# Optimization experiments

Hardware: AMD Instinct MI355X
Metric: run time of the kernel (lower is better)

## Reference

```python
import jax, jax.numpy as jnp
import numpy as np

EPS = 1e-5  # F.layer_norm default eps
H_STEP = 0.1


def double_layer(x, K1, K2):
    # x: [1, Cin, N]; K1: [Cmid, Cin]; K2: [Cout, Cmid]  (1x1 conv1d == matmul)
    x = jnp.einsum('oc,bcn->bon', K1, x)
    # F.layer_norm(x, x.shape): normalize over the whole tensor, no affine
    m = jnp.mean(x)
    v = jnp.mean((x - m) ** 2)
    x = jnp.tanh((x - m) * jax.lax.rsqrt(v + EPS))
    return jnp.einsum('oc,bcn->bon', K2, x)


def setup_inputs() -> dict:
    key = jax.random.key(0)
    ks = jax.random.split(key, 12)
    N = 4096; nNin = 64; nopen = 256; nhid = 256; nNclose = 256
    nlayer = 8; num_output = 1024; E0 = 16 * N
    stdv = 1e-3
    return {
        'xn': jax.random.normal(ks[0], (1, nNin, N), jnp.float32),
        'K1Nopen': jax.random.normal(ks[1], (nopen, nNin), jnp.float32) * stdv,
        'K2Nopen': jax.random.normal(ks[2], (nopen, nopen), jnp.float32) * stdv,
        'KNclose': jax.random.normal(ks[3], (nNclose, nopen), jnp.float32) * stdv,
        'KN1': jax.random.uniform(ks[4], (nlayer, nhid, 2 * nopen), jnp.float32) * stdv,
        'KN2': jax.random.uniform(ks[5], (nlayer, nopen, nhid), jnp.float32) * stdv,
        'lin1_w': jax.random.normal(ks[6], (nopen, nopen), jnp.float32) / np.sqrt(nopen),
        'lin1_b': jnp.zeros((nopen,), jnp.float32),
        'lin2_w': jax.random.normal(ks[7], (num_output, nopen), jnp.float32) / np.sqrt(nopen),
        'lin2_b': jnp.zeros((num_output,), jnp.float32),
        'edge_i': jax.random.randint(ks[8], (E0,), 0, N),
        'edge_j': jax.random.randint(ks[9], (E0,), 0, N),
    }


def reference(xn, K1Nopen, K2Nopen, KNclose, KN1, KN2,
              lin1_w, lin1_b, lin2_w, lin2_b, edge_i, edge_j):
    N = xn.shape[-1]
    # gcn_norm's add_remaining_self_loops: input edge list has no self loops,
    # so append one per node once (fixed shapes; D[i,i] == exp(0) == 1 == fill).
    I = jnp.concatenate([edge_i, jnp.arange(N)])
    J = jnp.concatenate([edge_j, jnp.arange(N)])

    xn = double_layer(xn, K1Nopen, K2Nopen)  # [1, nopen, N]
    nlayers = KN1.shape[0]
    for i in range(nlayers):
        # --- updateGraph: dense pairwise Gaussian affinity, then gcn_norm ---
        f = xn[0]                          # [C, N]
        sq = jnp.sum(f * f, axis=0)        # [N]
        D = jax.nn.relu(sq[None, :] + sq[:, None] - 2.0 * (f.T @ f))  # [N, N]
        D = jnp.exp(-2.0 * (D / jnp.std(D, ddof=1)))
        w = D[I, J]                                          # gather edge affinities
        deg = jax.ops.segment_sum(w, J, num_segments=N)
        dis = jnp.where(deg > 0, jax.lax.rsqrt(deg), 0.0)
        W = dis[I] * w * dis[J]                              # normalized edge weights [E]
        # --- nodeLap = edgeDiv(nodeGrad(xn)) ---
        g = W[None, None, :] * (xn[:, :, I] - xn[:, :, J])   # nodeGrad [1, C, E]
        wg = (W[None, None, :] * g)[0].T                     # [E, C]
        lap = (jax.ops.segment_sum(wg, I, num_segments=N)
               - jax.ops.segment_sum(wg, J, num_segments=N)).T[None]  # [1, C, N]
        dxn = jnp.concatenate([xn, lap], axis=1)             # varlet features [1, 2C, N]
        dxn = double_layer(dxn, KN1[i], KN2[i])              # [1, C, N]
        xn = xn + H_STEP * dxn                               # heat update

    xn = jnp.einsum('oc,bcn->bon', KNclose, xn)[0].T         # [N, nNclose]
    x = jax.nn.elu(xn @ lin1_w.T + lin1_b)
    x = x @ lin2_w.T + lin2_b
    return jax.nn.log_softmax(x, axis=1)                     # [N, num_output]
```

## Files before the change

### kernel.cpp

```cpp
#include <hip/hip_runtime.h>
#include <hip/hip_bf16.h>

#define N_NODES 4096
#define CF      256
#define CIN     64
#define E0_EDGES 65536
#define NLAYER  8
#define NOUT    1024
#define CN      (CF * N_NODES)
#define STD_BLOCKS 64

typedef unsigned short ushort;
typedef __attribute__((ext_vector_type(8))) short s8v;
typedef __attribute__((ext_vector_type(4))) float f4v;

__device__ __forceinline__ ushort f2bf(float x){
  unsigned int u = __builtin_bit_cast(unsigned int, x);
  return (ushort)((u + 0x7FFFu + ((u >> 16) & 1u)) >> 16);
}
__device__ __forceinline__ float bf2f(ushort h){
  unsigned int u = ((unsigned int)h) << 16;
  return __builtin_bit_cast(float, u);
}

__device__ __forceinline__ float waveSumF(float v){
  #pragma unroll
  for (int o = 32; o; o >>= 1) v += __shfl_xor(v, o);
  return v;
}
__device__ __forceinline__ double waveSumD(double v){
  #pragma unroll
  for (int o = 32; o; o >>= 1) v += __shfl_xor(v, o);
  return v;
}
__device__ __forceinline__ float waveMaxF(float v){
  #pragma unroll
  for (int o = 32; o; o >>= 1) v = fmaxf(v, __shfl_xor(v, o));
  return v;
}
__device__ float blockSumF(float v){
  __shared__ float sm[4];
  v = waveSumF(v);
  int l = threadIdx.x & 63, w = threadIdx.x >> 6;
  __syncthreads();
  if (l == 0) sm[w] = v;
  __syncthreads();
  return sm[0] + sm[1] + sm[2] + sm[3];
}
__device__ double blockSumD(double v){
  __shared__ double sm[4];
  v = waveSumD(v);
  int l = threadIdx.x & 63, w = threadIdx.x >> 6;
  __syncthreads();
  if (l == 0) sm[w] = v;
  __syncthreads();
  return sm[0] + sm[1] + sm[2] + sm[3];
}
__device__ float blockMaxF(float v){
  __shared__ float sm[4];
  v = waveMaxF(v);
  int l = threadIdx.x & 63, w = threadIdx.x >> 6;
  __syncthreads();
  if (l == 0) sm[w] = v;
  __syncthreads();
  return fmaxf(fmaxf(sm[0], sm[1]), fmaxf(sm[2], sm[3]));
}

#define MF(a,b,c) c = __builtin_amdgcn_mfma_f32_16x16x32_bf16(a, b, c, 0, 0, 0)

template<int BK, int ACT, bool WF32, bool WBF, bool WFH, bool MV, bool TRI>
__global__ __launch_bounds__(256)
void gemmB1(const ushort* __restrict__ A1, const ushort* __restrict__ A2,
            int lda, int splitAt,
            const ushort* __restrict__ B, int ldb,
            float* __restrict__ Cf, ushort* __restrict__ Cb, ushort* __restrict__ Cfh,
            int ldc, size_t cStrideZ, int kChunk,
            float alpha, float beta, const float* __restrict__ bias,
            double* __restrict__ pS, double* __restrict__ pS2)
{
  constexpr int NC = BK / 32;
  __shared__ ushort As[2][64][BK + 8], Bs[2][64][BK + 8];
  const int tid = threadIdx.x;
  const int r  = tid >> 2;
  const int kq = (tid & 3) * (BK / 4);
  int bx = blockIdx.x, by = blockIdx.y;
  if (TRI) {
    const int trT[10] = {0,0,0,0,1,1,1,2,2,3};
    const int tcT[10] = {0,1,2,3,1,2,3,2,3,3};
    by = trT[blockIdx.x]; bx = tcT[blockIdx.x];
  }
  const int row0 = by * 64, col0 = bx * 64;
  const int kStart = blockIdx.z * kChunk;
  const int nT = kChunk / BK;

  const int wid = tid >> 6, lane = tid & 63;
  const int wr = (wid >> 1) * 32, wc = (wid & 1) * 32;
  const int fr = lane & 15, fk = (lane >> 4) * 8;

  f4v acc[2][2] = {};
  s8v rA0[NC], rB0[NC], rA1[NC], rB1[NC];

#define LOADTILE(T, RA, RB) { \
    int k0 = kStart + (T) * BK; \
    const ushort* Ag; int kk; \
    if (k0 < splitAt) { Ag = A1; kk = k0; } else { Ag = A2; kk = k0 - splitAt; } \
    size_t aoff = (size_t)(row0 + r) * lda + kk + kq; \
    size_t boff = (size_t)(col0 + r) * ldb + k0 + kq; \
    _Pragma("unroll") \
    for (int c = 0; c < NC; c++) { \
      RA[c] = *(const s8v*)(Ag + aoff + 8 * c); \
      RB[c] = *(const s8v*)(B + boff + 8 * c); } }

#define STORETILE(BUF, RA, RB) { \
    _Pragma("unroll") \
    for (int c = 0; c < NC; c++) { \
      *(s8v*)&As[BUF][r][kq + 8 * c] = RA[c]; \
      *(s8v*)&Bs[BUF][r][kq + 8 * c] = RB[c]; } }

#define MFMAT(BUF) { \
    _Pragma("unroll") \
    for (int ks = 0; ks < BK; ks += 32) { \
      s8v a0 = *(const s8v*)&As[BUF][wr + fr][ks + fk]; \
      s8v a1 = *(const s8v*)&As[BUF][wr + 16 + fr][ks + fk]; \
      s8v b0 = *(const s8v*)&Bs[BUF][wc + fr][ks + fk]; \
      s8v b1 = *(const s8v*)&Bs[BUF][wc + 16 + fr][ks + fk]; \
      MF(a0, b0, acc[0][0]); \
      MF(a0, b1, acc[0][1]); \
      MF(a1, b0, acc[1][0]); \
      MF(a1, b1, acc[1][1]); } }

  LOADTILE(0, rA0, rB0);
  if (nT > 1) LOADTILE(1, rA1, rB1);
  STORETILE(0, rA0, rB0);

  for (int t = 0; t < nT; t += 2) {
    __syncthreads();
    if (t + 2 < nT) LOADTILE(t + 2, rA0, rB0);
    MFMAT(0);
    if (t + 1 < nT) {
      STORETILE(1, rA1, rB1);
      __syncthreads();
      if (t + 3 < nT) LOADTILE(t + 3, rA1, rB1);
      MFMAT(1);
      if (t + 2 < nT) STORETILE(0, rA0, rB0);
    }
  }
#undef LOADTILE
#undef STORETILE
#undef MFMAT

  double s = 0, s2 = 0;
  #pragma unroll
  for (int m = 0; m < 2; m++)
    #pragma unroll
    for (int n = 0; n < 2; n++) {
      const int rowb = row0 + wr + m * 16 + (lane >> 4) * 4;
      const int col  = col0 + wc + n * 16 + fr;
      ushort4 hv;
      #pragma unroll
      for (int q = 0; q < 4; q++) {
        size_t cidx = (size_t)(rowb + q) * ldc + col;
        float v = alpha * acc[m][n][q];
        if (cStrideZ) {
          Cf[blockIdx.z * cStrideZ + cidx] = v;
        } else {
          if (beta != 0.0f) v += beta * Cf[cidx];
          if (bias) v += bias[col];
          if (ACT == 1) v = (v > 0.0f) ? v : expm1f(v);
          if (WF32) Cf[cidx] = v;
          if (WBF)  Cb[cidx] = f2bf(v);
          if (WFH)  ((ushort*)&hv)[q] = f2bf(v);
          if (MV)   { s += v; s2 += (double)v * v; }
        }
      }
      if (WFH && !cStrideZ)
        *(ushort4*)(Cfh + (size_t)col * N_NODES + rowb) = hv;
    }
  if (MV) {
    s  = blockSumD(s);
    s2 = blockSumD(s2);
    if (tid == 0) {
      int bid = blockIdx.y * gridDim.x + blockIdx.x;
      pS[bid] = s; pS2[bid] = s2;
    }
  }
}

#define OFF_K1   0
#define OFF_K2   16384
#define OFF_KNC  81920
#define OFF_KN1  147456
#define OFF_KN2  1196032
#define OFF_L1   1720320
#define OFF_L2   1785856
#define NW_TOT   2048000

__global__ __launch_bounds__(256)
void prepWK(const float* s0, const float* s1, const float* s2, const float* s3,
            const float* s4, const float* s5, const float* s6,
            ushort* __restrict__ h)
{
  const int sizes[7] = {16384, 65536, 65536, 1048576, 524288, 65536, 262144};
  const int offs[7]  = {OFF_K1, OFF_K2, OFF_KNC, OFF_KN1, OFF_KN2, OFF_L1, OFF_L2};
  int seg = blockIdx.y;
  const float* src = seg==0?s0: seg==1?s1: seg==2?s2: seg==3?s3: seg==4?s4: seg==5?s5: s6;
  int n = sizes[seg], off = offs[seg];
  for (int i = blockIdx.x * 256 + threadIdx.x; i < n; i += gridDim.x * 256)
    h[off + i] = f2bf(src[i]);
}

__global__ __launch_bounds__(256)
void transposeBF(const float* __restrict__ in, ushort* __restrict__ outh, int R, int Cc)
{
  __shared__ float t[32][33];
  int x  = blockIdx.x * 32 + threadIdx.x;
  int y0 = blockIdx.y * 32;
  for (int dy = threadIdx.y; dy < 32; dy += 8)
    t[dy][threadIdx.x] = in[(size_t)(y0 + dy) * Cc + x];
  __syncthreads();
  int ox  = y0 + threadIdx.x;
  int oy0 = blockIdx.x * 32;
  for (int dy = threadIdx.y; dy < 32; dy += 8)
    outh[(size_t)(oy0 + dy) * R + ox] = f2bf(t[threadIdx.x][dy]);
}

__global__ __launch_bounds__(256)
void tanhNormBF(ushort* __restrict__ h, const double* __restrict__ pS,
                const double* __restrict__ pS2)
{
  __shared__ float bc[2];
  double a = pS[threadIdx.x], b = pS2[threadIdx.x];
  a = blockSumD(a);
  b = blockSumD(b);
  if (threadIdx.x == 0) {
    double m   = a / (double)CN;
    double var = b / (double)CN - m * m;
    bc[0] = (float)m;
    bc[1] = (float)(1.0 / sqrt(var + 1e-5));
  }
  __syncthreads();
  float mf = bc[0], rs = bc[1];
  for (size_t i = ((size_t)blockIdx.x * 256 + threadIdx.x) * 8; i < CN;
       i += (size_t)256 * 256 * 8) {
    s8v hv = *(s8v*)(h + i);
    #pragma unroll
    for (int k = 0; k < 8; k++) {
      float x = bf2f((ushort)hv[k]);
      x = tanhf((x - mf) * rs);
      hv[k] = (short)f2bf(x);
    }
    *(s8v*)(h + i) = hv;
  }
}

__global__ __launch_bounds__(256)
void sqSHK(const ushort* __restrict__ fTh, float* __restrict__ sq,
           float* __restrict__ sP, float* __restrict__ hP, float* __restrict__ deg)
{
  __shared__ float smS[4][256], smH[4][256];
  int b = blockIdx.x, w = threadIdx.x >> 6, lane = threadIdx.x & 63;
  if (threadIdx.x < 64) deg[b * 64 + threadIdx.x] = 0.0f;
  float sA[4] = {0,0,0,0}, hA[4] = {0,0,0,0};
  for (int rr = 0; rr < 16; rr++) {
    int n = b * 64 + rr * 4 + w;
    ushort4 u = ((const ushort4*)(fTh + (size_t)n * CF))[lane];
    float x0 = bf2f(u.x), x1 = bf2f(u.y), x2 = bf2f(u.z), x3 = bf2f(u.w);
    float q = waveSumF(x0*x0 + x1*x1 + x2*x2 + x3*x3);
    if (lane == 0) sq[n] = q;
    sA[0] += x0; sA[1] += x1; sA[2] += x2; sA[3] += x3;
    hA[0] += x0*q; hA[1] += x1*q; hA[2] += x2*q; hA[3] += x3*q;
  }
  #pragma unroll
  for (int k = 0; k < 4; k++) { smS[w][lane*4+k] = sA[k]; smH[w][lane*4+k] = hA[k]; }
  __syncthreads();
  int t = threadIdx.x;
  sP[(size_t)b * 256 + t] = smS[0][t] + smS[1][t] + smS[2][t] + smS[3][t];
  hP[(size_t)b * 256 + t] = smH[0][t] + smH[1][t] + smH[2][t] + smH[3][t];
}

__global__ __launch_bounds__(256)
void stdPartsK(const float* __restrict__ sP, const float* __restrict__ hP,
               const float* __restrict__ Gp, const float* __restrict__ sq,
               double* __restrict__ parts)
{
  int b = blockIdx.x, t = threadIdx.x;
  double S1 = 0, S2 = 0, sd = 0, hd = 0, gf = 0;
  for (int i = b * 256 + t; i < N_NODES; i += STD_BLOCKS * 256) {
    double q = sq[i]; S1 += q; S2 += q * q;
  }
  if (b == 0) {
    float sv = 0, hv = 0;
    for (int p = 0; p < 64; p++) { sv += sP[p * 256 + t]; hv += hP[p * 256 + t]; }
    sd = (double)sv * sv; hd = (double)hv * sv;
  }
  for (int i = b * 256 + t; i < CF * CF; i += STD_BLOCKS * 256) {
    int r = i >> 8, c = i & 255;
    if (r > c) continue;
    double g = 0;
    #pragma unroll 4
    for (int z = 0; z < 16; z++) g += Gp[(size_t)z * 65536 + i];
    gf += (r == c) ? g * g : 2.0 * g * g;
  }
  S1 = blockSumD(S1);
  S2 = blockSumD(S2);
  sd = blockSumD(sd);
  hd = blockSumD(hd);
  gf = blockSumD(gf);
  if (t == 0) {
    parts[0 * STD_BLOCKS + b] = S1;
    parts[1 * STD_BLOCKS + b] = S2;
    parts[2 * STD_BLOCKS + b] = sd;
    parts[3 * STD_BLOCKS + b] = hd;
    parts[4 * STD_BLOCKS + b] = gf;
  }
}

__global__ __launch_bounds__(256)
void edgeWK(const int* __restrict__ ei, const int* __restrict__ ej,
            const ushort* __restrict__ fTh, const float* __restrict__ sq,
            const double* __restrict__ parts, float* __restrict__ wE,
            float* __restrict__ deg)
{
  __shared__ float c0s;
  if (threadIdx.x < 64) {
    int l = threadIdx.x;
    double v0 = waveSumD(parts[0 * STD_BLOCKS + l]);
    double v1 = waveSumD(parts[1 * STD_BLOCKS + l]);
    double v2 = waveSumD(parts[2 * STD_BLOCKS + l]);
    double v3 = waveSumD(parts[3 * STD_BLOCKS + l]);
    double v4 = waveSumD(parts[4 * STD_BLOCKS + l]);
    if (l == 0) {
      double NN = (double)N_NODES;
      double sum1 = 2.0 * NN * v0 - 2.0 * v2;
      double sum2 = 2.0 * NN * v1 + 2.0 * v0 * v0 + 4.0 * v4 - 8.0 * v3;
      double n2 = NN * NN;
      double var = (sum2 - sum1 * sum1 / n2) / (n2 - 1.0);
      double sdev = sqrt(var > 0 ? var : 0);
      c0s = (float)(-2.0 / sdev);
    }
  }
  __syncthreads();
  float c0 = c0s;
  int w = threadIdx.x >> 6, lane = threadIdx.x & 63;
  int e0 = (blockIdx.x * 4 + w) * 4;
  for (int q = 0; q < 4; q++) {
    int e = e0 + q;
    int i = ei[e], j = ej[e];
    ushort4 ua = ((const ushort4*)(fTh + (size_t)i * CF))[lane];
    ushort4 ub = ((const ushort4*)(fTh + (size_t)j * CF))[lane];
    float d = waveSumF(bf2f(ua.x)*bf2f(ub.x) + bf2f(ua.y)*bf2f(ub.y) +
                       bf2f(ua.z)*bf2f(ub.z) + bf2f(ua.w)*bf2f(ub.w));
    if (lane == 0) {
      float dist = fmaxf(sq[i] + sq[j] - 2.0f * d, 0.0f);
      float ww = expf(c0 * dist);
      wE[e] = ww;
      unsafeAtomicAdd(&deg[j], ww);
    }
  }
}

__global__ __launch_bounds__(256)
void wsqK(const int* __restrict__ ei, const int* __restrict__ ej,
          const float* __restrict__ wE, const float* __restrict__ deg,
          float* __restrict__ Wsq)
{
  int e = blockIdx.x * 256 + threadIdx.x;
  float W = rsqrtf(1.0f + deg[ei[e]]) * wE[e] * rsqrtf(1.0f + deg[ej[e]]);
  Wsq[e] = W * W;
}

__global__ __launch_bounds__(256)
void csrCountK(const int* __restrict__ ei, const int* __restrict__ ej,
               int* __restrict__ cntO, int* __restrict__ cntI)
{
  int e = blockIdx.x * 256 + threadIdx.x;
  atomicAdd(&cntO[ei[e]], 1);
  atomicAdd(&cntI[ej[e]], 1);
}

__global__ __launch_bounds__(256)
void csrScanK(const int* __restrict__ cntO, const int* __restrict__ cntI,
              int* __restrict__ ofsO, int* __restrict__ ofsI)
{
  __shared__ int smO[256], smI[256];
  int t = threadIdx.x;
  int lo[16], li[16];
  int sO = 0, sI = 0;
  #pragma unroll
  for (int k = 0; k < 16; k++) {
    lo[k] = cntO[t * 16 + k]; li[k] = cntI[t * 16 + k];
    sO += lo[k]; sI += li[k];
  }
  smO[t] = sO; smI[t] = sI;
  __syncthreads();
  for (int off = 1; off < 256; off <<= 1) {
    int aO = (t >= off) ? smO[t - off] : 0;
    int aI = (t >= off) ? smI[t - off] : 0;
    __syncthreads();
    smO[t] += aO; smI[t] += aI;
    __syncthreads();
  }
  int bO = smO[t] - sO;
  int bI = smI[t] - sI;
  #pragma unroll
  for (int k = 0; k < 16; k++) {
    ofsO[t * 16 + k] = bO; bO += lo[k];
    ofsI[t * 16 + k] = bI; bI += li[k];
  }
}

__global__ __launch_bounds__(256)
void csrFillK(const int* __restrict__ ei, const int* __restrict__ ej,
              const int* __restrict__ ofsO, const int* __restrict__ ofsI,
              int* __restrict__ curO, int* __restrict__ curI,
              int2* __restrict__ lstO, int2* __restrict__ lstI)
{
  int e = blockIdx.x * 256 + threadIdx.x;
  int i = ei[e], j = ej[e];
  int p = atomicAdd(&curO[i], 1); lstO[ofsO[i] + p] = make_int2(j, e);
  int q = atomicAdd(&curI[j], 1); lstI[ofsI[j] + q] = make_int2(i, e);
}

__global__ __launch_bounds__(256)
void gatherLapK(const int2* __restrict__ lstO, const int2* __restrict__ lstI,
                const int* __restrict__ ofsO, const int* __restrict__ ofsI,
                const int* __restrict__ cntO, const int* __restrict__ cntI,
                const float* __restrict__ Wsq,
                const ushort* __restrict__ fTh, ushort* __restrict__ lapTh)
{
  int w = threadIdx.x >> 6, lane = threadIdx.x & 63;
  int n = blockIdx.x * 4 + w;
  ushort4 u = ((const ushort4*)(fTh + (size_t)n * CF))[lane];
  float o0 = bf2f(u.x), o1 = bf2f(u.y), o2 = bf2f(u.z), o3 = bf2f(u.w);
  float a0 = 0, a1 = 0, a2 = 0, a3 = 0;
  int p0 = ofsO[n], pc = cntO[n];
  for (int k = 0; k < pc; k++) {
    int2 oe = lstO[p0 + k];
    float W2 = Wsq[oe.y];
    ushort4 v = ((const ushort4*)(fTh + (size_t)oe.x * CF))[lane];
    a0 += W2 * (o0 - bf2f(v.x)); a1 += W2 * (o1 - bf2f(v.y));
    a2 += W2 * (o2 - bf2f(v.z)); a3 += W2 * (o3 - bf2f(v.w));
  }
  int q0 = ofsI[n], qc = cntI[n];
  for (int k = 0; k < qc; k++) {
    int2 oe = lstI[q0 + k];
    float W2 = Wsq[oe.y];
    ushort4 v = ((const ushort4*)(fTh + (size_t)oe.x * CF))[lane];
    a0 += W2 * (o0 - bf2f(v.x)); a1 += W2 * (o1 - bf2f(v.y));
    a2 += W2 * (o2 - bf2f(v.z)); a3 += W2 * (o3 - bf2f(v.w));
  }
  ushort4 rv;
  rv.x = f2bf(a0); rv.y = f2bf(a1); rv.z = f2bf(a2); rv.w = f2bf(a3);
  ((ushort4*)(lapTh + (size_t)n * CF))[lane] = rv;
}

__global__ __launch_bounds__(256)
void logSoftmaxK(const float* __restrict__ logits, float* __restrict__ out)
{
  int n = blockIdx.x;
  const float* row = logits + (size_t)n * NOUT;
  float mx = -1e30f;
  for (int o = threadIdx.x; o < NOUT; o += 256) mx = fmaxf(mx, row[o]);
  mx = blockMaxF(mx);
  float se = 0;
  for (int o = threadIdx.x; o < NOUT; o += 256) se += expf(row[o] - mx);
  se = blockSumF(se);
  float lse = mx + logf(se);
  for (int o = threadIdx.x; o < NOUT; o += 256) out[(size_t)n * NOUT + o] = row[o] - lse;
}

extern "C" void kernel_launch(void* const* d_in, const int* in_sizes, int n_in,
                              void* d_out, int out_size, void* d_ws, size_t ws_size,
                              hipStream_t stream)
{
  (void)in_sizes; (void)n_in; (void)out_size; (void)ws_size;
  const float* x0      = (const float*)d_in[0];
  const float* K1      = (const float*)d_in[1];
  const float* K2      = (const float*)d_in[2];
  const float* KNclose = (const float*)d_in[3];
  const float* KN1     = (const float*)d_in[4];
  const float* KN2     = (const float*)d_in[5];
  const float* lin1w   = (const float*)d_in[6];
  const float* lin1b   = (const float*)d_in[7];
  const float* lin2w   = (const float*)d_in[8];
  const float* lin2b   = (const float*)d_in[9];
  const int*   ei      = (const int*)d_in[10];
  const int*   ej      = (const int*)d_in[11];
  float* out = (float*)d_out;

  float* base   = (float*)d_ws;
  float* fT     = base;
  float* logits = fT + (size_t)CN;
  float* Gp     = logits + 4 * (size_t)CN;
  float* sq     = Gp + (size_t)CN;
  float* deg    = sq + N_NODES;
  float* sP     = deg + N_NODES;
  float* hP     = sP + 64 * 256;
  float* wE     = hP + 64 * 256;
  float* Wsq    = wE + E0_EDGES;
  double* pS    = (double*)(Wsq + E0_EDGES + 2);
  double* pS2   = pS + 256;
  double* parts = pS2 + 256;

  ushort* u0 = (ushort*)(((uintptr_t)(parts + 5 * STD_BLOCKS) + 15) & ~(uintptr_t)15);
  ushort* fTh   = u0;
  ushort* fh    = fTh + (size_t)CN;
  ushort* lapTh = fh + (size_t)CN;
  ushort* uTh   = lapTh + (size_t)CN;
  ushort* wH    = uTh + (size_t)CN;
  int* ib = (int*)(((uintptr_t)(wH + NW_TOT) + 15) & ~(uintptr_t)15);
  int*  cntO = ib;
  int*  cntI = cntO + N_NODES;
  int*  ofsO = cntI + N_NODES;
  int*  ofsI = ofsO + N_NODES;
  int*  curO = ofsI + N_NODES;
  int*  curI = curO + N_NODES;
  int2* lstO = (int2*)(curI + N_NODES);
  int2* lstI = lstO + E0_EDGES;

  prepWK<<<dim3(64, 7), 256, 0, stream>>>(K1, K2, KNclose, KN1, KN2, lin1w, lin2w, wH);
  hipMemsetAsync(cntO, 0, 6 * N_NODES * sizeof(int), stream);
  csrCountK<<<E0_EDGES/256, 256, 0, stream>>>(ei, ej, cntO, cntI);
  csrScanK<<<1, 256, 0, stream>>>(cntO, cntI, ofsO, ofsI);
  csrFillK<<<E0_EDGES/256, 256, 0, stream>>>(ei, ej, ofsO, ofsI, curO, curI, lstO, lstI);

  transposeBF<<<dim3(N_NODES/32, CIN/32), dim3(32, 8), 0, stream>>>(x0, fh, CIN, N_NODES);
  gemmB1<64,0,0,1,0,1,false><<<dim3(4,64,1), 256, 0, stream>>>(
      fh, fh, CIN, 1 << 30, wH + OFF_K1, CIN,
      nullptr, uTh, nullptr, CF, 0, CIN, 1.f, 0.f, nullptr, pS, pS2);
  tanhNormBF<<<256, 256, 0, stream>>>(uTh, pS, pS2);
  gemmB1<128,0,1,1,1,0,false><<<dim3(4,64,1), 256, 0, stream>>>(
      uTh, uTh, CF, 1 << 30, wH + OFF_K2, CF,
      fT, fTh, fh, CF, 0, CF, 1.f, 0.f, nullptr, nullptr, nullptr);

  for (int L = 0; L < NLAYER; L++) {
    const ushort* k1h = wH + OFF_KN1 + (size_t)L * CF * 2 * CF;
    const ushort* k2h = wH + OFF_KN2 + (size_t)L * CF * CF;

    sqSHK<<<64, 256, 0, stream>>>(fTh, sq, sP, hP, deg);
    gemmB1<128,0,1,0,0,0,true><<<dim3(10,1,16), 256, 0, stream>>>(
        fh, fh, N_NODES, 1 << 30, fh, N_NODES,
        Gp, nullptr, nullptr, CF, 65536, 256, 1.f, 0.f, nullptr, nullptr, nullptr);
    stdPartsK<<<STD_BLOCKS, 256, 0, stream>>>(sP, hP, Gp, sq, parts);
    edgeWK<<<E0_EDGES/16, 256, 0, stream>>>(ei, ej, fTh, sq, parts, wE, deg);
    wsqK<<<E0_EDGES/256, 256, 0, stream>>>(ei, ej, wE, deg, Wsq);
    gatherLapK<<<N_NODES/4, 256, 0, stream>>>(lstO, lstI, ofsO, ofsI, cntO, cntI,
                                              Wsq, fTh, lapTh);
    gemmB1<128,0,0,1,0,1,false><<<dim3(4,64,1), 256, 0, stream>>>(
        fTh, lapTh, CF, 256, k1h, 2*CF,
        nullptr, uTh, nullptr, CF, 0, 2*CF, 1.f, 0.f, nullptr, pS, pS2);
    tanhNormBF<<<256, 256, 0, stream>>>(uTh, pS, pS2);
    gemmB1<128,0,1,1,1,0,false><<<dim3(4,64,1), 256, 0, stream>>>(
        uTh, uTh, CF, 1 << 30, k2h, CF,
        fT, fTh, fh, CF, 0, CF, 0.1f, 1.f, nullptr, nullptr, nullptr);
  }

  gemmB1<128,0,0,1,0,0,false><<<dim3(4,64,1), 256, 0, stream>>>(
      fTh, fTh, CF, 1 << 30, wH + OFF_KNC, CF,
      nullptr, uTh, nullptr, CF, 0, CF, 1.f, 0.f, nullptr, nullptr, nullptr);
  gemmB1<128,1,0,1,0,0,false><<<dim3(4,64,1), 256, 0, stream>>>(
      uTh, uTh, CF, 1 << 30, wH + OFF_L1, CF,
      nullptr, lapTh, nullptr, CF, 0, CF, 1.f, 0.f, lin1b, nullptr, nullptr);
  gemmB1<128,0,1,0,0,0,false><<<dim3(16,64,1), 256, 0, stream>>>(
      lapTh, lapTh, CF, 1 << 30, wH + OFF_L2, CF,
      logits, nullptr, nullptr, NOUT, 0, CF, 1.f, 0.f, lin2b, nullptr, nullptr);
  logSoftmaxK<<<N_NODES, 256, 0, stream>>>(logits, out);
}
```

Before: 820.7 us.

## Fuse tanh-norm into GEMM load, atomic split-K Gram, coarser edge kernel

Removes the standalone tanhNormBF pass by applying the layer-norm tanh while staging A tiles into shared memory of the following GEMM; each block recomputes mean/var from the partial sums. The split-K Gram GEMM now accumulates into a single 256x256 buffer with atomics (zeroed in sqSHK) instead of writing 16 partial slabs that stdPartsK summed. The edge weight kernel processes 16 edges per wave with fewer blocks. Tradeoffs: tanh is recomputed for each column tile (4x redundancy), atomics make the sum order nondeterministic, and edgeWK has less parallelism.

```diff
diff --git a/kernel.cpp b/kernel.cpp
--- a/kernel.cpp
+++ b/kernel.cpp
@@ -68,7 +68,8 @@
 
 #define MF(a,b,c) c = __builtin_amdgcn_mfma_f32_16x16x32_bf16(a, b, c, 0, 0, 0)
 
-template<int BK, int ACT, bool WF32, bool WBF, bool WFH, bool MV, bool TRI>
+template<int BK, int ACT, bool WF32, bool WBF, bool WFH, bool MV, bool TRI,
+         bool TANH, bool ATO>
 __global__ __launch_bounds__(256)
 void gemmB1(const ushort* __restrict__ A1, const ushort* __restrict__ A2,
             int lda, int splitAt,
@@ -97,6 +98,17 @@
   const int wr = (wid >> 1) * 32, wc = (wid & 1) * 32;
   const int fr = lane & 15, fk = (lane >> 4) * 8;
 
+  float mf = 0.0f, rs = 0.0f;
+  if (TANH) {
+    double a = pS[tid], b = pS2[tid];
+    a = blockSumD(a);
+    b = blockSumD(b);
+    double m   = a / (double)CN;
+    double var = b / (double)CN - m * m;
+    mf = (float)m;
+    rs = (float)(1.0 / sqrt(var + 1e-5));
+  }
+
   f4v acc[2][2] = {};
   s8v rA0[NC], rB0[NC], rA1[NC], rB1[NC];
 
@@ -114,7 +126,13 @@
 #define STORETILE(BUF, RA, RB) { \
     _Pragma("unroll") \
     for (int c = 0; c < NC; c++) { \
-      *(s8v*)&As[BUF][r][kq + 8 * c] = RA[c]; \
+      s8v av = RA[c]; \
+      if (TANH) { \
+        _Pragma("unroll") \
+        for (int k2 = 0; k2 < 8; k2++) { \
+          float x = bf2f((ushort)av[k2]); \
+          av[k2] = (short)f2bf(tanhf((x - mf) * rs)); } } \
+      *(s8v*)&As[BUF][r][kq + 8 * c] = av; \
       *(s8v*)&Bs[BUF][r][kq + 8 * c] = RB[c]; } }
 
 #define MFMAT(BUF) { \
@@ -161,7 +179,9 @@
       for (int q = 0; q < 4; q++) {
         size_t cidx = (size_t)(rowb + q) * ldc + col;
         float v = alpha * acc[m][n][q];
-        if (cStrideZ) {
+        if (ATO) {
+          unsafeAtomicAdd(&Cf[cidx], v);
+        } else if (cStrideZ) {
           Cf[blockIdx.z * cStrideZ + cidx] = v;
         } else {
           if (beta != 0.0f) v += beta * Cf[cidx];
@@ -173,7 +193,7 @@
           if (MV)   { s += v; s2 += (double)v * v; }
         }
       }
-      if (WFH && !cStrideZ)
+      if (WFH && !cStrideZ && !ATO)
         *(ushort4*)(Cfh + (size_t)col * N_NODES + rowb) = hv;
     }
   if (MV) {
@@ -225,41 +245,14 @@
 }
 
 __global__ __launch_bounds__(256)
-void tanhNormBF(ushort* __restrict__ h, const double* __restrict__ pS,
-                const double* __restrict__ pS2)
-{
-  __shared__ float bc[2];
-  double a = pS[threadIdx.x], b = pS2[threadIdx.x];
-  a = blockSumD(a);
-  b = blockSumD(b);
-  if (threadIdx.x == 0) {
-    double m   = a / (double)CN;
-    double var = b / (double)CN - m * m;
-    bc[0] = (float)m;
-    bc[1] = (float)(1.0 / sqrt(var + 1e-5));
-  }
-  __syncthreads();
-  float mf = bc[0], rs = bc[1];
-  for (size_t i = ((size_t)blockIdx.x * 256 + threadIdx.x) * 8; i < CN;
-       i += (size_t)256 * 256 * 8) {
-    s8v hv = *(s8v*)(h + i);
-    #pragma unroll
-    for (int k = 0; k < 8; k++) {
-      float x = bf2f((ushort)hv[k]);
-      x = tanhf((x - mf) * rs);
-      hv[k] = (short)f2bf(x);
-    }
-    *(s8v*)(h + i) = hv;
-  }
-}
-
-__global__ __launch_bounds__(256)
 void sqSHK(const ushort* __restrict__ fTh, float* __restrict__ sq,
-           float* __restrict__ sP, float* __restrict__ hP, float* __restrict__ deg)
+           float* __restrict__ sP, float* __restrict__ hP,
+           float* __restrict__ deg, float* __restrict__ G)
 {
   __shared__ float smS[4][256], smH[4][256];
   int b = blockIdx.x, w = threadIdx.x >> 6, lane = threadIdx.x & 63;
   if (threadIdx.x < 64) deg[b * 64 + threadIdx.x] = 0.0f;
+  ((float4*)G)[b * 256 + threadIdx.x] = make_float4(0.f, 0.f, 0.f, 0.f);
   float sA[4] = {0,0,0,0}, hA[4] = {0,0,0,0};
   for (int rr = 0; rr < 16; rr++) {
     int n = b * 64 + rr * 4 + w;
@@ -280,7 +273,7 @@
 
 __global__ __launch_bounds__(256)
 void stdPartsK(const float* __restrict__ sP, const float* __restrict__ hP,
-               const float* __restrict__ Gp, const float* __restrict__ sq,
+               const float* __restrict__ G, const float* __restrict__ sq,
                double* __restrict__ parts)
 {
   int b = blockIdx.x, t = threadIdx.x;
@@ -296,9 +289,7 @@
   for (int i = b * 256 + t; i < CF * CF; i += STD_BLOCKS * 256) {
     int r = i >> 8, c = i & 255;
     if (r > c) continue;
-    double g = 0;
-    #pragma unroll 4
-    for (int z = 0; z < 16; z++) g += Gp[(size_t)z * 65536 + i];
+    double g = G[i];
     gf += (r == c) ? g * g : 2.0 * g * g;
   }
   S1 = blockSumD(S1);
@@ -342,8 +333,8 @@
   __syncthreads();
   float c0 = c0s;
   int w = threadIdx.x >> 6, lane = threadIdx.x & 63;
-  int e0 = (blockIdx.x * 4 + w) * 4;
-  for (int q = 0; q < 4; q++) {
+  int e0 = (blockIdx.x * 4 + w) * 16;
+  for (int q = 0; q < 16; q++) {
     int e = e0 + q;
     int i = ei[e], j = ej[e];
     ushort4 ua = ((const ushort4*)(fTh + (size_t)i * CF))[lane];
@@ -491,8 +482,8 @@
   float* base   = (float*)d_ws;
   float* fT     = base;
   float* logits = fT + (size_t)CN;
-  float* Gp     = logits + 4 * (size_t)CN;
-  float* sq     = Gp + (size_t)CN;
+  float* G      = logits + 4 * (size_t)CN;
+  float* sq     = G + CF * CF;
   float* deg    = sq + N_NODES;
   float* sP     = deg + N_NODES;
   float* hP     = sP + 64 * 256;
@@ -525,43 +516,41 @@
   csrFillK<<<E0_EDGES/256, 256, 0, stream>>>(ei, ej, ofsO, ofsI, curO, curI, lstO, lstI);
 
   transposeBF<<<dim3(N_NODES/32, CIN/32), dim3(32, 8), 0, stream>>>(x0, fh, CIN, N_NODES);
-  gemmB1<64,0,0,1,0,1,false><<<dim3(4,64,1), 256, 0, stream>>>(
+  gemmB1<64,0,0,1,0,1,false,false,false><<<dim3(4,64,1), 256, 0, stream>>>(
       fh, fh, CIN, 1 << 30, wH + OFF_K1, CIN,
       nullptr, uTh, nullptr, CF, 0, CIN, 1.f, 0.f, nullptr, pS, pS2);
-  tanhNormBF<<<256, 256, 0, stream>>>(uTh, pS, pS2);
-  gemmB1<128,0,1,1,1,0,false><<<dim3(4,64,1), 256, 0, stream>>>(
+  gemmB1<128,0,1,1,1,0,false,true,false><<<dim3(4,64,1), 256, 0, stream>>>(
       uTh, uTh, CF, 1 << 30, wH + OFF_K2, CF,
-      fT, fTh, fh, CF, 0, CF, 1.f, 0.f, nullptr, nullptr, nullptr);
+      fT, fTh, fh, CF, 0, CF, 1.f, 0.f, nullptr, pS, pS2);
 
   for (int L = 0; L < NLAYER; L++) {
     const ushort* k1h = wH + OFF_KN1 + (size_t)L * CF * 2 * CF;
     const ushort* k2h = wH + OFF_KN2 + (size_t)L * CF * CF;
 
-    sqSHK<<<64, 256, 0, stream>>>(fTh, sq, sP, hP, deg);
-    gemmB1<128,0,1,0,0,0,true><<<dim3(10,1,16), 256, 0, stream>>>(
+    sqSHK<<<64, 256, 0, stream>>>(fTh, sq, sP, hP, deg, G);
+    gemmB1<128,0,0,0,0,0,true,false,true><<<dim3(10,1,16), 256, 0, stream>>>(
         fh, fh, N_NODES, 1 << 30, fh, N_NODES,
-        Gp, nullptr, nullptr, CF, 65536, 256, 1.f, 0.f, nullptr, nullptr, nullptr);
-    stdPartsK<<<STD_BLOCKS, 256, 0, stream>>>(sP, hP, Gp, sq, parts);
-    edgeWK<<<E0_EDGES/16, 256, 0, stream>>>(ei, ej, fTh, sq, parts, wE, deg);
+        G, nullptr, nullptr, CF, 0, 256, 1.f, 0.f, nullptr, nullptr, nullptr);
+    stdPartsK<<<STD_BLOCKS, 256, 0, stream>>>(sP, hP, G, sq, parts);
+    edgeWK<<<E0_EDGES/64, 256, 0, stream>>>(ei, ej, fTh, sq, parts, wE, deg);
     wsqK<<<E0_EDGES/256, 256, 0, stream>>>(ei, ej, wE, deg, Wsq);
     gatherLapK<<<N_NODES/4, 256, 0, stream>>>(lstO, lstI, ofsO, ofsI, cntO, cntI,
                                               Wsq, fTh, lapTh);
-    gemmB1<128,0,0,1,0,1,false><<<dim3(4,64,1), 256, 0, stream>>>(
+    gemmB1<128,0,0,1,0,1,false,false,false><<<dim3(4,64,1), 256, 0, stream>>>(
         fTh, lapTh, CF, 256, k1h, 2*CF,
         nullptr, uTh, nullptr, CF, 0, 2*CF, 1.f, 0.f, nullptr, pS, pS2);
-    tanhNormBF<<<256, 256, 0, stream>>>(uTh, pS, pS2);
-    gemmB1<128,0,1,1,1,0,false><<<dim3(4,64,1), 256, 0, stream>>>(
+    gemmB1<128,0,1,1,1,0,false,true,false><<<dim3(4,64,1), 256, 0, stream>>>(
         uTh, uTh, CF, 1 << 30, k2h, CF,
-        fT, fTh, fh, CF, 0, CF, 0.1f, 1.f, nullptr, nullptr, nullptr);
-  }
-
-  gemmB1<128,0,0,1,0,0,false><<<dim3(4,64,1), 256, 0, stream>>>(
+        fT, fTh, fh, CF, 0, CF, 0.1f, 1.f, nullptr, pS, pS2);
+  }
+
+  gemmB1<128,0,0,1,0,0,false,false,false><<<dim3(4,64,1), 256, 0, stream>>>(
       fTh, fTh, CF, 1 << 30, wH + OFF_KNC, CF,
       nullptr, uTh, nullptr, CF, 0, CF, 1.f, 0.f, nullptr, nullptr, nullptr);
-  gemmB1<128,1,0,1,0,0,false><<<dim3(4,64,1), 256, 0, stream>>>(
+  gemmB1<128,1,0,1,0,0,false,false,false><<<dim3(4,64,1), 256, 0, stream>>>(
       uTh, uTh, CF, 1 << 30, wH + OFF_L1, CF,
       nullptr, lapTh, nullptr, CF, 0, CF, 1.f, 0.f, lin1b, nullptr, nullptr);
-  gemmB1<128,0,1,0,0,0,false><<<dim3(16,64,1), 256, 0, stream>>>(
+  gemmB1<128,0,1,0,0,0,false,false,false><<<dim3(16,64,1), 256, 0, stream>>>(
       lapTh, lapTh, CF, 1 << 30, wH + OFF_L2, CF,
       logits, nullptr, nullptr, NOUT, 0, CF, 1.f, 0.f, lin2b, nullptr, nullptr);
   logSoftmaxK<<<N_NODES, 256, 0, stream>>>(logits, out);
```

Result: slower. 881.4 us (+7.4%).
